# Optimization experiments

Measured on AMD Instinct MI355X. Metric: run time of the kernel, lower is better.

The kernel has to match this reference:

```python
import jax, jax.numpy as jnp
import numpy as np

LATENT = 32
GRID = 32
G1 = GRID + 1  # 33 samples per axis (align_corners grid)
HID = 128
N_POINTS = 1048576


def _trilinear_sample(emb, points):
    """Faithful F.grid_sample(mode='bilinear', padding_mode='zeros', align_corners=True).
    emb: [(G1)^3, C] flat table; points: [n,3] in [-1,1], (x,y,z) -> (W,H,D)."""
    C = emb.shape[1]
    # torch .view(1, C, D, H, W) on the flat [(G1)^3 * C] buffer: same reshape here.
    vol = emb.reshape(C, G1, G1, G1).transpose(1, 2, 3, 0)  # [D, H, W, C]
    # align_corners=True: u in [-1,1] -> pixel coord (u+1)/2 * (size-1)
    coords = (points + 1.0) * (0.5 * (G1 - 1))
    x, y, z = coords[:, 0], coords[:, 1], coords[:, 2]
    x0 = jnp.floor(x); y0 = jnp.floor(y); z0 = jnp.floor(z)
    fx = x - x0; fy = y - y0; fz = z - z0
    x0i = x0.astype(jnp.int32); y0i = y0.astype(jnp.int32); z0i = z0.astype(jnp.int32)
    x1i = x0i + 1; y1i = y0i + 1; z1i = z0i + 1

    def corner(zi, yi, xi, w):
        valid = ((zi >= 0) & (zi < G1) & (yi >= 0) & (yi < G1)
                 & (xi >= 0) & (xi < G1))
        zc = jnp.clip(zi, 0, G1 - 1)
        yc = jnp.clip(yi, 0, G1 - 1)
        xc = jnp.clip(xi, 0, G1 - 1)
        v = vol[zc, yc, xc]  # [n, C] gather
        return v * (w * valid.astype(w.dtype))[:, None]

    wx0, wx1 = 1.0 - fx, fx
    wy0, wy1 = 1.0 - fy, fy
    wz0, wz1 = 1.0 - fz, fz
    lat = (corner(z0i, y0i, x0i, wz0 * wy0 * wx0)
           + corner(z0i, y0i, x1i, wz0 * wy0 * wx1)
           + corner(z0i, y1i, x0i, wz0 * wy1 * wx0)
           + corner(z0i, y1i, x1i, wz0 * wy1 * wx1)
           + corner(z1i, y0i, x0i, wz1 * wy0 * wx0)
           + corner(z1i, y0i, x1i, wz1 * wy0 * wx1)
           + corner(z1i, y1i, x0i, wz1 * wy1 * wx0)
           + corner(z1i, y1i, x1i, wz1 * wy1 * wx1))
    return lat  # [n, C]


def setup_inputs() -> dict:
    key = jax.random.key(0)
    ks = jax.random.split(key, 8)
    points = jax.random.uniform(ks[0], (N_POINTS, 3), dtype=jnp.float32)  # in [0,1) subset of [-1,1]
    emb = jax.random.normal(ks[1], (G1 ** 3, LATENT), dtype=jnp.float32)
    w1 = jax.random.normal(ks[2], (LATENT, HID), dtype=jnp.float32) * 0.05
    b1 = jax.random.normal(ks[3], (HID,), dtype=jnp.float32) * 0.05
    w2 = jax.random.normal(ks[4], (HID, HID), dtype=jnp.float32) * 0.05
    b2 = jax.random.normal(ks[5], (HID,), dtype=jnp.float32) * 0.05
    w3 = jax.random.normal(ks[6], (HID, 1), dtype=jnp.float32) * 0.05
    b3 = jax.random.normal(ks[7], (1,), dtype=jnp.float32) * 0.05
    return {"points": points, "emb": emb, "w1": w1, "b1": b1,
            "w2": w2, "b2": b2, "w3": w3, "b3": b3}


def reference(points, emb, w1, b1, w2, b2, w3, b3):
    lat = _trilinear_sample(emb, points)                # [n, latent]
    h = jax.nn.relu(lat @ w1 + b1)                      # [n, hid]
    h = jax.nn.relu(h @ w2 + b2)                        # [n, hid]
    sdf = jnp.tanh(h @ w3 + b3)                         # [n, 1]
    return sdf
```

## Files before the change

kernel.cpp:

```cpp
#include <hip/hip_runtime.h>
#include <hip/hip_bf16.h>

#define NPTS 1048576
#define G1I  33
#define NV   35937
#define NC   32
#define HIDD 128

typedef _Float16 h8  __attribute__((ext_vector_type(8)));
typedef __fp16   p2  __attribute__((ext_vector_type(2)));
typedef float    f4  __attribute__((ext_vector_type(4)));

#define AS_GLOBAL(p) ((const __attribute__((address_space(1))) char*)(p))
#define AS_LDS(p)    ((__attribute__((address_space(3))) char*)(p))

#define WS_A1  0
#define WS_A2  8192
#define WS_A3  40960
#define WS_EMB 65536
#define WS_NEED (WS_EMB + NV*NC*2)


__global__ __launch_bounds__(256) void vox_prep(
    const float* __restrict__ emb, const float* __restrict__ w1,
    const float* __restrict__ w2, const float* __restrict__ w3,
    char* __restrict__ ws)
{
    __shared__ _Float16 tile[256][NC];
    const int b = blockIdx.x, t = threadIdx.x;
    _Float16* embh = (_Float16*)(ws + WS_EMB);
    if (b < 141) {
        const int v = b*256 + t;
        #pragma unroll
        for (int c = 0; c < NC; ++c) {
            float val = (v < NV) ? emb[c*NV + v] : 0.f;
            const int pos = ((c & 12) << 1) | (c & 3) | ((c >> 4) << 2);
            tile[t][pos] = (_Float16)val;
        }
        __syncthreads();
        if (v < NV) {
            uint4* dst = (uint4*)(embh + v*NC);
            const uint4* src = (const uint4*)&tile[t][0];
            #pragma unroll
            for (int j = 0; j < 4; ++j) dst[j] = src[j];
        }
    } else if (b < 149) {
        const int t2 = b - 141;
        const int ks = t >> 6, l = t & 63;
        const int gq = l >> 4, colh = l & 15;
        _Float16* a2f = (_Float16*)(ws + WS_A2);
        h8 fr;
        #pragma unroll
        for (int i = 0; i < 8; ++i) {
            const int k = 32*ks + 16*(i>>2) + 4*gq + (i&3);
            fr[i] = (_Float16)w2[k*HIDD + 16*t2 + colh];
        }
        *(h8*)(a2f + ((t2*4+ks)*64 + l)*8) = fr;
    } else if (b == 149) {
        _Float16* a1f = (_Float16*)(ws + WS_A1);
        #pragma unroll
        for (int it = 0; it < 2; ++it) {
            const int item = t + it*256;
            const int t8 = item >> 6, l = item & 63;
            const int gq = l >> 4, colh = l & 15;
            h8 fr;
            #pragma unroll
            for (int i = 0; i < 8; ++i) {
                const int k = 16*(i>>2) + 4*gq + (i&3);
                fr[i] = (_Float16)w1[k*HIDD + 16*t8 + colh];
            }
            *(h8*)(a1f + (t8*64 + l)*8) = fr;
        }
    } else {
        _Float16* a3f = (_Float16*)(ws + WS_A3);
        const int j = t >> 6, l = t & 63;
        const int gq = l >> 4;
        h8 fr;
        #pragma unroll
        for (int i = 0; i < 8; ++i) {
            const int k = 32*j + 16*(i>>2) + 4*gq + (i&3);
            fr[i] = (_Float16)w3[k];
        }
        *(h8*)(a3f + (j*64 + l)*8) = fr;
    }
}

__global__ __launch_bounds__(512) void vox_main(
    const float* __restrict__ points, const char* __restrict__ ws,
    const float* __restrict__ b1, const float* __restrict__ b2,
    const float* __restrict__ b3v, float* __restrict__ out)
{
    __shared__ _Float16 latl[512][40];
    __shared__ uint4    a2l[2048];

    const int tid  = threadIdx.x;
    const int lane = tid & 63;
    const int wv   = tid >> 6;
    const int gq   = lane >> 4;
    const int colh = lane & 15;

    {
        const uint4* a2g = (const uint4*)(ws + WS_A2);
        #pragma unroll
        for (int j = 0; j < 4; ++j) {
            const uint4* gsrc = a2g + (j*512 + tid);
            uint4*       ldst = ((uint4*)a2l) + (j*512 + wv*64);
            __builtin_amdgcn_global_load_lds(
                (const __attribute__((address_space(1))) void*)AS_GLOBAL(gsrc),
                (__attribute__((address_space(3))) void*)AS_LDS(ldst),
                16, 0, 0);
        }
    }

    const char* embB = (const char*)(ws + WS_EMB);
    const int p = blockIdx.x*512 + tid;
    const float px = points[3*p+0], py = points[3*p+1], pz = points[3*p+2];
    const float xc = (px + 1.f)*16.f, yc = (py + 1.f)*16.f, zc = (pz + 1.f)*16.f;
    const float xf = floorf(xc), yf = floorf(yc), zf = floorf(zc);
    const float fx = xc - xf, fy = yc - yf, fz = zc - zf;
    const int vb = (((int)zf)*G1I + (int)yf)*G1I + (int)xf;

    const int q  = lane >> 2;
    const int ch = lane & 3;
    h8 accch[4];
    #pragma unroll
    for (int sh = 0; sh < 4; ++sh) {
        const int s = sh*16 + q;
        const float fxs = __shfl(fx, s);
        const float fys = __shfl(fy, s);
        const float fzs = __shfl(fz, s);
        const int   vbs = __shfl(vb, s);
        const char* bz0 = embB + (size_t)((unsigned)vbs*64u + (unsigned)ch*16u);
        const char* bz1 = bz0 + 69696;
        const h8 v0 = *(const h8*)(bz0 +    0);
        const h8 v1 = *(const h8*)(bz0 +   64);
        const h8 v2 = *(const h8*)(bz0 + 2112);
        const h8 v3 = *(const h8*)(bz0 + 2176);
        const h8 v4 = *(const h8*)(bz1 +    0);
        const h8 v5 = *(const h8*)(bz1 +   64);
        const h8 v6 = *(const h8*)(bz1 + 2112);
        const h8 v7 = *(const h8*)(bz1 + 2176);
        const float wx1 = fxs, wx0 = 1.f - fxs;
        const float wy1 = fys, wy0 = 1.f - fys;
        const float wz1 = fzs, wz0 = 1.f - fzs;
        h8 a = (h8){0,0,0,0,0,0,0,0};
        {
            const _Float16 w0 = (_Float16)(wz0*wy0*wx0); const h8 W0 = {w0,w0,w0,w0,w0,w0,w0,w0}; a += W0*v0;
            const _Float16 w1_ = (_Float16)(wz0*wy0*wx1); const h8 W1 = {w1_,w1_,w1_,w1_,w1_,w1_,w1_,w1_}; a += W1*v1;
            const _Float16 w2_ = (_Float16)(wz0*wy1*wx0); const h8 W2 = {w2_,w2_,w2_,w2_,w2_,w2_,w2_,w2_}; a += W2*v2;
            const _Float16 w3_ = (_Float16)(wz0*wy1*wx1); const h8 W3 = {w3_,w3_,w3_,w3_,w3_,w3_,w3_,w3_}; a += W3*v3;
            const _Float16 w4_ = (_Float16)(wz1*wy0*wx0); const h8 W4 = {w4_,w4_,w4_,w4_,w4_,w4_,w4_,w4_}; a += W4*v4;
            const _Float16 w5_ = (_Float16)(wz1*wy0*wx1); const h8 W5 = {w5_,w5_,w5_,w5_,w5_,w5_,w5_,w5_}; a += W5*v5;
            const _Float16 w6_ = (_Float16)(wz1*wy1*wx0); const h8 W6 = {w6_,w6_,w6_,w6_,w6_,w6_,w6_,w6_}; a += W6*v6;
            const _Float16 w7_ = (_Float16)(wz1*wy1*wx1); const h8 W7 = {w7_,w7_,w7_,w7_,w7_,w7_,w7_,w7_}; a += W7*v7;
        }
        accch[sh] = a;
    }
    #pragma unroll
    for (int sh = 0; sh < 4; ++sh)
        *(uint4*)&latl[wv*64 + sh*16 + q][8*ch] = *(uint4*)&accch[sh];
    asm volatile("s_waitcnt lgkmcnt(0)" ::: "memory");

    const h8* a1g = (const h8*)(ws + WS_A1);
    h8 a1fr[8];
    #pragma unroll
    for (int t8 = 0; t8 < 8; ++t8) a1fr[t8] = a1g[t8*64 + lane];

    h8 B2f[4][4];
    #pragma unroll
    for (int pt = 0; pt < 4; ++pt) {
        const h8 bf = *(const h8*)&latl[wv*64 + pt*16 + colh][8*gq];
        f4 acc1[8];
        #pragma unroll
        for (int t8 = 0; t8 < 8; ++t8) acc1[t8] = *(const f4*)(b1 + 16*t8 + 4*gq);
        #pragma unroll
        for (int t8 = 0; t8 < 8; ++t8)
            acc1[t8] = __builtin_amdgcn_mfma_f32_16x16x32_f16(a1fr[t8], bf, acc1[t8], 0, 0, 0);
        #pragma unroll
        for (int ks = 0; ks < 4; ++ks) {
            union { h8 v; p2 h[4]; } u;
            const p2 z = {(__fp16)0, (__fp16)0};
            u.h[0] = __builtin_elementwise_max(__builtin_amdgcn_cvt_pkrtz(acc1[2*ks  ][0], acc1[2*ks  ][1]), z);
            u.h[1] = __builtin_elementwise_max(__builtin_amdgcn_cvt_pkrtz(acc1[2*ks  ][2], acc1[2*ks  ][3]), z);
            u.h[2] = __builtin_elementwise_max(__builtin_amdgcn_cvt_pkrtz(acc1[2*ks+1][0], acc1[2*ks+1][1]), z);
            u.h[3] = __builtin_elementwise_max(__builtin_amdgcn_cvt_pkrtz(acc1[2*ks+1][2], acc1[2*ks+1][3]), z);
            B2f[pt][ks] = u.v;
        }
    }

    asm volatile("s_waitcnt vmcnt(0)" ::: "memory");
    __syncthreads();

    const h8* a3g = (const h8*)(ws + WS_A3);
    f4 acc3[4];
    #pragma unroll
    for (int pt = 0; pt < 4; ++pt) acc3[pt] = (f4){0.f,0.f,0.f,0.f};
    #pragma unroll
    for (int q2 = 0; q2 < 4; ++q2) {
        const f4 b2e = *(const f4*)(b2 + 16*(2*q2  ) + 4*gq);
        const f4 b2o = *(const f4*)(b2 + 16*(2*q2+1) + 4*gq);
        f4 acc2e[4], acc2o[4];
        #pragma unroll
        for (int pt = 0; pt < 4; ++pt) { acc2e[pt] = b2e; acc2o[pt] = b2o; }
        #pragma unroll
        for (int ks = 0; ks < 4; ++ks) {
            const h8 fe = *(const h8*)&a2l[((2*q2  )*4 + ks)*64 + lane];
            #pragma unroll
            for (int pt = 0; pt < 4; ++pt)
                acc2e[pt] = __builtin_amdgcn_mfma_f32_16x16x32_f16(fe, B2f[pt][ks], acc2e[pt], 0, 0, 0);
        }
        #pragma unroll
        for (int ks = 0; ks < 4; ++ks) {
            const h8 fo = *(const h8*)&a2l[((2*q2+1)*4 + ks)*64 + lane];
            #pragma unroll
            for (int pt = 0; pt < 4; ++pt)
                acc2o[pt] = __builtin_amdgcn_mfma_f32_16x16x32_f16(fo, B2f[pt][ks], acc2o[pt], 0, 0, 0);
        }
        const h8 a3fr = a3g[q2*64 + lane];
        #pragma unroll
        for (int pt = 0; pt < 4; ++pt) {
            union { h8 v; p2 h[4]; } u;
            const p2 z = {(__fp16)0, (__fp16)0};
            u.h[0] = __builtin_elementwise_max(__builtin_amdgcn_cvt_pkrtz(acc2e[pt][0], acc2e[pt][1]), z);
            u.h[1] = __builtin_elementwise_max(__builtin_amdgcn_cvt_pkrtz(acc2e[pt][2], acc2e[pt][3]), z);
            u.h[2] = __builtin_elementwise_max(__builtin_amdgcn_cvt_pkrtz(acc2o[pt][0], acc2o[pt][1]), z);
            u.h[3] = __builtin_elementwise_max(__builtin_amdgcn_cvt_pkrtz(acc2o[pt][2], acc2o[pt][3]), z);
            acc3[pt] = __builtin_amdgcn_mfma_f32_16x16x32_f16(a3fr, u.v, acc3[pt], 0, 0, 0);
        }
    }

    float sv = 0.f;
    #pragma unroll
    for (int pt = 0; pt < 4; ++pt) if (gq == pt) sv = acc3[pt][0];
    const float zi = sv + b3v[0];
    const float e  = __expf(2.f*zi);
    out[blockIdx.x*512 + tid] = (e - 1.f) / (e + 1.f);
}

extern "C" void kernel_launch(void* const* d_in, const int* in_sizes, int n_in,
                              void* d_out, int out_size, void* d_ws, size_t ws_size,
                              hipStream_t stream)
{
    const float* points = (const float*)d_in[0];
    const float* emb    = (const float*)d_in[1];
    const float* w1     = (const float*)d_in[2];
    const float* b1     = (const float*)d_in[3];
    const float* w2     = (const float*)d_in[4];
    const float* b2     = (const float*)d_in[5];
    const float* w3     = (const float*)d_in[6];
    const float* b3     = (const float*)d_in[7];
    float* out = (float*)d_out;
    char*  ws  = (char*)d_ws;
    if (ws_size < (size_t)WS_NEED) return;

    hipLaunchKernelGGL(vox_prep, dim3(151), dim3(256), 0, stream, emb, w1, w2, w3, ws);
    hipLaunchKernelGGL(vox_main, dim3(NPTS/512), dim3(512), 0, stream,
                       points, ws, b1, b2, b3, out);
}
```

Measured before the change: 132.1 us.

## Split per-wave point processing into two passes to cut register pressure

Each wave now handles its 64 points in two passes of 32: gather plus layer 1 for two 16-point tiles, then layers 2 and 3, then repeat. Live B2f fragments and accumulators are halved, the LDS latent staging buffer shrinks to half, and launch bounds request 4 blocks per CU so more waves can be resident to hide gather latency. Points are loaded directly per subgroup instead of being shuffled. In exchange, the second gather can no longer overlap with the first pass's MLP within a wave, and the weight fragments are reused across two passes.

New measurement: 139.7 us. 1.06x slower.

```diff
diff --git a/kernel.cpp b/kernel.cpp
--- a/kernel.cpp
+++ b/kernel.cpp
@@ -85,12 +85,12 @@
     }
 }
 
-__global__ __launch_bounds__(512) void vox_main(
+__global__ __launch_bounds__(512, 4) void vox_main(
     const float* __restrict__ points, const char* __restrict__ ws,
     const float* __restrict__ b1, const float* __restrict__ b2,
     const float* __restrict__ b3v, float* __restrict__ out)
 {
-    __shared__ _Float16 latl[512][40];
+    __shared__ _Float16 latl[256][40];
     __shared__ uint4    a2l[2048];
 
     const int tid  = threadIdx.x;
@@ -98,6 +98,8 @@
     const int wv   = tid >> 6;
     const int gq   = lane >> 4;
     const int colh = lane & 15;
+    const int q    = lane >> 2;
+    const int ch   = lane & 3;
 
     {
         const uint4* a2g = (const uint4*)(ws + WS_A2);
@@ -113,125 +115,132 @@
     }
 
     const char* embB = (const char*)(ws + WS_EMB);
-    const int p = blockIdx.x*512 + tid;
-    const float px = points[3*p+0], py = points[3*p+1], pz = points[3*p+2];
-    const float xc = (px + 1.f)*16.f, yc = (py + 1.f)*16.f, zc = (pz + 1.f)*16.f;
-    const float xf = floorf(xc), yf = floorf(yc), zf = floorf(zc);
-    const float fx = xc - xf, fy = yc - yf, fz = zc - zf;
-    const int vb = (((int)zf)*G1I + (int)yf)*G1I + (int)xf;
-
-    const int q  = lane >> 2;
-    const int ch = lane & 3;
-    h8 accch[4];
+    const int sgbase = blockIdx.x*512 + wv*64 + q;
+    float px4[4], py4[4], pz4[4];
     #pragma unroll
     for (int sh = 0; sh < 4; ++sh) {
-        const int s = sh*16 + q;
-        const float fxs = __shfl(fx, s);
-        const float fys = __shfl(fy, s);
-        const float fzs = __shfl(fz, s);
-        const int   vbs = __shfl(vb, s);
-        const char* bz0 = embB + (size_t)((unsigned)vbs*64u + (unsigned)ch*16u);
-        const char* bz1 = bz0 + 69696;
-        const h8 v0 = *(const h8*)(bz0 +    0);
-        const h8 v1 = *(const h8*)(bz0 +   64);
-        const h8 v2 = *(const h8*)(bz0 + 2112);
-        const h8 v3 = *(const h8*)(bz0 + 2176);
-        const h8 v4 = *(const h8*)(bz1 +    0);
-        const h8 v5 = *(const h8*)(bz1 +   64);
-        const h8 v6 = *(const h8*)(bz1 + 2112);
-        const h8 v7 = *(const h8*)(bz1 + 2176);
-        const float wx1 = fxs, wx0 = 1.f - fxs;
-        const float wy1 = fys, wy0 = 1.f - fys;
-        const float wz1 = fzs, wz0 = 1.f - fzs;
-        h8 a = (h8){0,0,0,0,0,0,0,0};
-        {
-            const _Float16 w0 = (_Float16)(wz0*wy0*wx0); const h8 W0 = {w0,w0,w0,w0,w0,w0,w0,w0}; a += W0*v0;
-            const _Float16 w1_ = (_Float16)(wz0*wy0*wx1); const h8 W1 = {w1_,w1_,w1_,w1_,w1_,w1_,w1_,w1_}; a += W1*v1;
-            const _Float16 w2_ = (_Float16)(wz0*wy1*wx0); const h8 W2 = {w2_,w2_,w2_,w2_,w2_,w2_,w2_,w2_}; a += W2*v2;
-            const _Float16 w3_ = (_Float16)(wz0*wy1*wx1); const h8 W3 = {w3_,w3_,w3_,w3_,w3_,w3_,w3_,w3_}; a += W3*v3;
-            const _Float16 w4_ = (_Float16)(wz1*wy0*wx0); const h8 W4 = {w4_,w4_,w4_,w4_,w4_,w4_,w4_,w4_}; a += W4*v4;
-            const _Float16 w5_ = (_Float16)(wz1*wy0*wx1); const h8 W5 = {w5_,w5_,w5_,w5_,w5_,w5_,w5_,w5_}; a += W5*v5;
-            const _Float16 w6_ = (_Float16)(wz1*wy1*wx0); const h8 W6 = {w6_,w6_,w6_,w6_,w6_,w6_,w6_,w6_}; a += W6*v6;
-            const _Float16 w7_ = (_Float16)(wz1*wy1*wx1); const h8 W7 = {w7_,w7_,w7_,w7_,w7_,w7_,w7_,w7_}; a += W7*v7;
-        }
-        accch[sh] = a;
-    }
-    #pragma unroll
-    for (int sh = 0; sh < 4; ++sh)
-        *(uint4*)&latl[wv*64 + sh*16 + q][8*ch] = *(uint4*)&accch[sh];
-    asm volatile("s_waitcnt lgkmcnt(0)" ::: "memory");
+        const float* pp = points + 3*(sgbase + sh*16);
+        px4[sh] = pp[0]; py4[sh] = pp[1]; pz4[sh] = pp[2];
+    }
 
     const h8* a1g = (const h8*)(ws + WS_A1);
     h8 a1fr[8];
     #pragma unroll
     for (int t8 = 0; t8 < 8; ++t8) a1fr[t8] = a1g[t8*64 + lane];
 
-    h8 B2f[4][4];
-    #pragma unroll
-    for (int pt = 0; pt < 4; ++pt) {
-        const h8 bf = *(const h8*)&latl[wv*64 + pt*16 + colh][8*gq];
-        f4 acc1[8];
-        #pragma unroll
-        for (int t8 = 0; t8 < 8; ++t8) acc1[t8] = *(const f4*)(b1 + 16*t8 + 4*gq);
-        #pragma unroll
-        for (int t8 = 0; t8 < 8; ++t8)
-            acc1[t8] = __builtin_amdgcn_mfma_f32_16x16x32_f16(a1fr[t8], bf, acc1[t8], 0, 0, 0);
-        #pragma unroll
-        for (int ks = 0; ks < 4; ++ks) {
-            union { h8 v; p2 h[4]; } u;
-            const p2 z = {(__fp16)0, (__fp16)0};
-            u.h[0] = __builtin_elementwise_max(__builtin_amdgcn_cvt_pkrtz(acc1[2*ks  ][0], acc1[2*ks  ][1]), z);
-            u.h[1] = __builtin_elementwise_max(__builtin_amdgcn_cvt_pkrtz(acc1[2*ks  ][2], acc1[2*ks  ][3]), z);
-            u.h[2] = __builtin_elementwise_max(__builtin_amdgcn_cvt_pkrtz(acc1[2*ks+1][0], acc1[2*ks+1][1]), z);
-            u.h[3] = __builtin_elementwise_max(__builtin_amdgcn_cvt_pkrtz(acc1[2*ks+1][2], acc1[2*ks+1][3]), z);
-            B2f[pt][ks] = u.v;
-        }
-    }
-
+    const h8* a3g = (const h8*)(ws + WS_A3);
+    float sv = 0.f;
+    h8 B2f[2][4];
+
+#define GATHER_L1(PASS)                                                               \
+    {                                                                                 \
+        _Pragma("unroll")                                                             \
+        for (int shl = 0; shl < 2; ++shl) {                                           \
+            const int sh = (PASS)*2 + shl;                                            \
+            const float xc = (px4[sh] + 1.f)*16.f;                                    \
+            const float yc = (py4[sh] + 1.f)*16.f;                                    \
+            const float zc = (pz4[sh] + 1.f)*16.f;                                    \
+            const float xf = floorf(xc), yf = floorf(yc), zf = floorf(zc);            \
+            const float fxs = xc - xf, fys = yc - yf, fzs = zc - zf;                  \
+            const int vbs = (((int)zf)*G1I + (int)yf)*G1I + (int)xf;                  \
+            const char* bz0 = embB + (size_t)((unsigned)vbs*64u + (unsigned)ch*16u);  \
+            const char* bz1 = bz0 + 69696;                                            \
+            const h8 v0 = *(const h8*)(bz0 +    0);                                   \
+            const h8 v1 = *(const h8*)(bz0 +   64);                                   \
+            const h8 v2 = *(const h8*)(bz0 + 2112);                                   \
+            const h8 v3 = *(const h8*)(bz0 + 2176);                                   \
+            const h8 v4 = *(const h8*)(bz1 +    0);                                   \
+            const h8 v5 = *(const h8*)(bz1 +   64);                                   \
+            const h8 v6 = *(const h8*)(bz1 + 2112);                                   \
+            const h8 v7 = *(const h8*)(bz1 + 2176);                                   \
+            const float wx1 = fxs, wx0 = 1.f - fxs;                                   \
+            const float wy1 = fys, wy0 = 1.f - fys;                                   \
+            const float wz1 = fzs, wz0 = 1.f - fzs;                                   \
+            h8 a = (h8){0,0,0,0,0,0,0,0};                                             \
+            { const _Float16 w = (_Float16)(wz0*wy0*wx0); const h8 W={w,w,w,w,w,w,w,w}; a += W*v0; } \
+            { const _Float16 w = (_Float16)(wz0*wy0*wx1); const h8 W={w,w,w,w,w,w,w,w}; a += W*v1; } \
+            { const _Float16 w = (_Float16)(wz0*wy1*wx0); const h8 W={w,w,w,w,w,w,w,w}; a += W*v2; } \
+            { const _Float16 w = (_Float16)(wz0*wy1*wx1); const h8 W={w,w,w,w,w,w,w,w}; a += W*v3; } \
+            { const _Float16 w = (_Float16)(wz1*wy0*wx0); const h8 W={w,w,w,w,w,w,w,w}; a += W*v4; } \
+            { const _Float16 w = (_Float16)(wz1*wy0*wx1); const h8 W={w,w,w,w,w,w,w,w}; a += W*v5; } \
+            { const _Float16 w = (_Float16)(wz1*wy1*wx0); const h8 W={w,w,w,w,w,w,w,w}; a += W*v6; } \
+            { const _Float16 w = (_Float16)(wz1*wy1*wx1); const h8 W={w,w,w,w,w,w,w,w}; a += W*v7; } \
+            *(uint4*)&latl[wv*32 + shl*16 + q][8*ch] = *(uint4*)&a;                   \
+        }                                                                             \
+              \
+        asm volatile("s_waitcnt lgkmcnt(0)" ::: "memory");                            \
+        _Pragma("unroll")                                                             \
+        for (int ptl = 0; ptl < 2; ++ptl) {                                           \
+            const h8 bf = *(const h8*)&latl[wv*32 + ptl*16 + colh][8*gq];             \
+            _Pragma("unroll")                                                         \
+            for (int ks = 0; ks < 4; ++ks) {                                          \
+                f4 ae = *(const f4*)(b1 + 16*(2*ks  ) + 4*gq);                        \
+                f4 ao = *(const f4*)(b1 + 16*(2*ks+1) + 4*gq);                        \
+                ae = __builtin_amdgcn_mfma_f32_16x16x32_f16(a1fr[2*ks  ], bf, ae, 0, 0, 0); \
+                ao = __builtin_amdgcn_mfma_f32_16x16x32_f16(a1fr[2*ks+1], bf, ao, 0, 0, 0); \
+                union { h8 v; p2 h[4]; } u;                                           \
+                const p2 z = {(__fp16)0, (__fp16)0};                                  \
+                u.h[0] = __builtin_elementwise_max(__builtin_amdgcn_cvt_pkrtz(ae[0], ae[1]), z); \
+                u.h[1] = __builtin_elementwise_max(__builtin_amdgcn_cvt_pkrtz(ae[2], ae[3]), z); \
+                u.h[2] = __builtin_elementwise_max(__builtin_amdgcn_cvt_pkrtz(ao[0], ao[1]), z); \
+                u.h[3] = __builtin_elementwise_max(__builtin_amdgcn_cvt_pkrtz(ao[2], ao[3]), z); \
+                B2f[ptl][ks] = u.v;                                                   \
+            }                                                                         \
+        }                                                                             \
+    }
+
+#define L23(PASS)                                                                     \
+    {                                                                                 \
+        f4 acc3[2];                                                                   \
+        acc3[0] = (f4){0.f,0.f,0.f,0.f}; acc3[1] = (f4){0.f,0.f,0.f,0.f};             \
+        _Pragma("unroll")                                                             \
+        for (int q2 = 0; q2 < 4; ++q2) {                                              \
+            const f4 b2e = *(const f4*)(b2 + 16*(2*q2  ) + 4*gq);                     \
+            const f4 b2o = *(const f4*)(b2 + 16*(2*q2+1) + 4*gq);                     \
+            f4 a2e0 = b2e, a2e1 = b2e, a2o0 = b2o, a2o1 = b2o;                        \
+            _Pragma("unroll")                                                         \
+            for (int ks = 0; ks < 4; ++ks) {                                          \
+                const h8 fe = *(const h8*)&a2l[((2*q2  )*4 + ks)*64 + lane];          \
+                a2e0 = __builtin_amdgcn_mfma_f32_16x16x32_f16(fe, B2f[0][ks], a2e0, 0, 0, 0); \
+                a2e1 = __builtin_amdgcn_mfma_f32_16x16x32_f16(fe, B2f[1][ks], a2e1, 0, 0, 0); \
+            }                                                                         \
+            _Pragma("unroll")                                                         \
+            for (int ks = 0; ks < 4; ++ks) {                                          \
+                const h8 fo = *(const h8*)&a2l[((2*q2+1)*4 + ks)*64 + lane];          \
+                a2o0 = __builtin_amdgcn_mfma_f32_16x16x32_f16(fo, B2f[0][ks], a2o0, 0, 0, 0); \
+                a2o1 = __builtin_amdgcn_mfma_f32_16x16x32_f16(fo, B2f[1][ks], a2o1, 0, 0, 0); \
+            }                                                                         \
+            const h8 a3fr = a3g[q2*64 + lane];                                        \
+            {                                                                         \
+                union { h8 v; p2 h[4]; } u;                                           \
+                const p2 z = {(__fp16)0, (__fp16)0};                                  \
+                u.h[0] = __builtin_elementwise_max(__builtin_amdgcn_cvt_pkrtz(a2e0[0], a2e0[1]), z); \
+                u.h[1] = __builtin_elementwise_max(__builtin_amdgcn_cvt_pkrtz(a2e0[2], a2e0[3]), z); \
+                u.h[2] = __builtin_elementwise_max(__builtin_amdgcn_cvt_pkrtz(a2o0[0], a2o0[1]), z); \
+                u.h[3] = __builtin_elementwise_max(__builtin_amdgcn_cvt_pkrtz(a2o0[2], a2o0[3]), z); \
+                acc3[0] = __builtin_amdgcn_mfma_f32_16x16x32_f16(a3fr, u.v, acc3[0], 0, 0, 0); \
+            }                                                                         \
+            {                                                                         \
+                union { h8 v; p2 h[4]; } u;                                           \
+                const p2 z = {(__fp16)0, (__fp16)0};                                  \
+                u.h[0] = __builtin_elementwise_max(__builtin_amdgcn_cvt_pkrtz(a2e1[0], a2e1[1]), z); \
+                u.h[1] = __builtin_elementwise_max(__builtin_amdgcn_cvt_pkrtz(a2e1[2], a2e1[3]), z); \
+                u.h[2] = __builtin_elementwise_max(__builtin_amdgcn_cvt_pkrtz(a2o1[0], a2o1[1]), z); \
+                u.h[3] = __builtin_elementwise_max(__builtin_amdgcn_cvt_pkrtz(a2o1[2], a2o1[3]), z); \
+                acc3[1] = __builtin_amdgcn_mfma_f32_16x16x32_f16(a3fr, u.v, acc3[1], 0, 0, 0); \
+            }                                                                         \
+        }                                                                             \
+        if (gq == (PASS)*2 + 0) sv = acc3[0][0];                                      \
+        if (gq == (PASS)*2 + 1) sv = acc3[1][0];                                      \
+    }
+
+    GATHER_L1(0)
     asm volatile("s_waitcnt vmcnt(0)" ::: "memory");
     __syncthreads();
-
-    const h8* a3g = (const h8*)(ws + WS_A3);
-    f4 acc3[4];
-    #pragma unroll
-    for (int pt = 0; pt < 4; ++pt) acc3[pt] = (f4){0.f,0.f,0.f,0.f};
-    #pragma unroll
-    for (int q2 = 0; q2 < 4; ++q2) {
-        const f4 b2e = *(const f4*)(b2 + 16*(2*q2  ) + 4*gq);
-        const f4 b2o = *(const f4*)(b2 + 16*(2*q2+1) + 4*gq);
-        f4 acc2e[4], acc2o[4];
-        #pragma unroll
-        for (int pt = 0; pt < 4; ++pt) { acc2e[pt] = b2e; acc2o[pt] = b2o; }
-        #pragma unroll
-        for (int ks = 0; ks < 4; ++ks) {
-            const h8 fe = *(const h8*)&a2l[((2*q2  )*4 + ks)*64 + lane];
-            #pragma unroll
-            for (int pt = 0; pt < 4; ++pt)
-                acc2e[pt] = __builtin_amdgcn_mfma_f32_16x16x32_f16(fe, B2f[pt][ks], acc2e[pt], 0, 0, 0);
-        }
-        #pragma unroll
-        for (int ks = 0; ks < 4; ++ks) {
-            const h8 fo = *(const h8*)&a2l[((2*q2+1)*4 + ks)*64 + lane];
-            #pragma unroll
-            for (int pt = 0; pt < 4; ++pt)
-                acc2o[pt] = __builtin_amdgcn_mfma_f32_16x16x32_f16(fo, B2f[pt][ks], acc2o[pt], 0, 0, 0);
-        }
-        const h8 a3fr = a3g[q2*64 + lane];
-        #pragma unroll
-        for (int pt = 0; pt < 4; ++pt) {
-            union { h8 v; p2 h[4]; } u;
-            const p2 z = {(__fp16)0, (__fp16)0};
-            u.h[0] = __builtin_elementwise_max(__builtin_amdgcn_cvt_pkrtz(acc2e[pt][0], acc2e[pt][1]), z);
-            u.h[1] = __builtin_elementwise_max(__builtin_amdgcn_cvt_pkrtz(acc2e[pt][2], acc2e[pt][3]), z);
-            u.h[2] = __builtin_elementwise_max(__builtin_amdgcn_cvt_pkrtz(acc2o[pt][0], acc2o[pt][1]), z);
-            u.h[3] = __builtin_elementwise_max(__builtin_amdgcn_cvt_pkrtz(acc2o[pt][2], acc2o[pt][3]), z);
-            acc3[pt] = __builtin_amdgcn_mfma_f32_16x16x32_f16(a3fr, u.v, acc3[pt], 0, 0, 0);
-        }
-    }
-
-    float sv = 0.f;
-    #pragma unroll
-    for (int pt = 0; pt < 4; ++pt) if (gq == pt) sv = acc3[pt][0];
+    L23(0)
+    GATHER_L1(1)
+    L23(1)
+
     const float zi = sv + b3v[0];
     const float e  = __expf(2.f*zi);
     out[blockIdx.x*512 + tid] = (e - 1.f) / (e + 1.f);
```
